# Performance work log

Hardware: AMD Instinct MI355X
Metric: run time of the kernel (lower is better)

Reference implementation:

```python
import jax, jax.numpy as jnp
import numpy as np

H = 768
NH = 12
HD = H // NH
EPS = 1e-12


def setup_inputs() -> dict:
    key = jax.random.key(0)
    ks = jax.random.split(key, 12)
    B, S = 4, 1024
    scale = 0.02
    return {
        "hidden_states": jax.random.normal(ks[0], (B, S, H), jnp.float32),
        "rel_pos": jax.random.normal(ks[1], (B, NH, S, S), jnp.float32),
        "rel_2d_pos": jax.random.normal(ks[2], (B, NH, S, S), jnp.float32),
        "Wq": jax.random.normal(ks[3], (H, H), jnp.float32) * scale,
        "bq": jnp.zeros((H,), jnp.float32),
        "Wk": jax.random.normal(ks[4], (H, H), jnp.float32) * scale,
        "bk": jnp.zeros((H,), jnp.float32),
        "Wv": jax.random.normal(ks[5], (H, H), jnp.float32) * scale,
        "bv": jnp.zeros((H,), jnp.float32),
        "Wo": jax.random.normal(ks[6], (H, H), jnp.float32) * scale,
        "bo": jnp.zeros((H,), jnp.float32),
        "ln_g": jnp.ones((H,), jnp.float32),
        "ln_b": jnp.zeros((H,), jnp.float32),
    }


def reference(hidden_states, rel_pos, rel_2d_pos, Wq, bq, Wk, bk, Wv, bv, Wo, bo, ln_g, ln_b):
    B, S, _ = hidden_states.shape
    # qkv projections -> [B, S, NH, HD]
    q = (hidden_states @ Wq + bq).reshape(B, S, NH, HD)
    k = (hidden_states @ Wk + bk).reshape(B, S, NH, HD)
    v = (hidden_states @ Wv + bv).reshape(B, S, NH, HD)
    q = q / jnp.sqrt(jnp.asarray(HD, q.dtype))
    # attention scores [B, NH, S, S] + relative/spatial biases
    scores = jnp.einsum("bshd,bthd->bhst", q, k) + rel_pos + rel_2d_pos
    probs = jax.nn.softmax(scores.astype(jnp.float32), axis=-1).astype(v.dtype)
    # context [B, S, NH, HD] -> [B, S, H]
    ctx = jnp.einsum("bhst,bthd->bshd", probs, v).reshape(B, S, H)
    # self-output: dense + residual + LayerNorm
    y = ctx @ Wo + bo + hidden_states
    mu = jnp.mean(y, axis=-1, keepdims=True)
    var = jnp.mean((y - mu) ** 2, axis=-1, keepdims=True)
    out = (y - mu) * jax.lax.rsqrt(var + EPS) * ln_g + ln_b
    return out
```

## Files before the change

kernel.cpp:

```cpp
#include <hip/hip_runtime.h>

#define H 768
#define NH 12
#define HD 64
#define BB 4
#define SS 1024
#define MM (BB*SS)

typedef __bf16 bf16;
typedef __bf16 bf16x8 __attribute__((ext_vector_type(8)));
typedef __bf16 bf16x4 __attribute__((ext_vector_type(4)));
typedef float  f32x4  __attribute__((ext_vector_type(4)));

static __device__ __forceinline__ f32x4 mfma16(bf16x8 a, bf16x8 b, f32x4 c){
  return __builtin_amdgcn_mfma_f32_16x16x32_bf16(a, b, c, 0, 0, 0);
}

__global__ __launch_bounds__(256) void prep_hs(const float* __restrict__ hs, bf16* __restrict__ hsb){
  size_t i = (size_t)blockIdx.x*256 + threadIdx.x;
  f32x4 v = *(const f32x4*)(hs + i*4);
  bf16x4 o;
  #pragma unroll
  for(int j=0;j<4;j++) o[j] = (bf16)v[j];
  *(bf16x4*)(hsb + i*4) = o;
}

__global__ __launch_bounds__(256) void prep_wt(const float* __restrict__ Wq, const float* __restrict__ Wk,
                                               const float* __restrict__ Wv, const float* __restrict__ Wo,
                                               bf16* __restrict__ oq, bf16* __restrict__ ok,
                                               bf16* __restrict__ ov, bf16* __restrict__ oo){
  int z = blockIdx.z;
  const float* W = (z==0)?Wq:(z==1)?Wk:(z==2)?Wv:Wo;
  bf16* O = (z==0)?oq:(z==1)?ok:(z==2)?ov:oo;
  __shared__ float tile[64][65];
  int t = threadIdx.x;
  int k0 = blockIdx.y*64, n0 = blockIdx.x*64;
  #pragma unroll
  for(int i=0;i<4;i++){
    int idx = i*256+t; int r = idx>>4; int c4 = (idx&15)*4;
    f32x4 v = *(const f32x4*)(W + (size_t)(k0+r)*H + n0 + c4);
    tile[r][c4+0]=v[0]; tile[r][c4+1]=v[1]; tile[r][c4+2]=v[2]; tile[r][c4+3]=v[3];
  }
  __syncthreads();
  #pragma unroll
  for(int i=0;i<4;i++){
    int idx = i*256+t; int r = idx>>4; int c4 = (idx&15)*4;
    bf16x4 o;
    #pragma unroll
    for(int j=0;j<4;j++) o[j] = (bf16)tile[c4+j][r];
    *(bf16x4*)(O + (size_t)(n0+r)*H + k0 + c4) = o;
  }
}

__global__ __launch_bounds__(256) void qkv_gemm(const bf16* __restrict__ hsb,
    const bf16* __restrict__ wqT, const bf16* __restrict__ wkT, const bf16* __restrict__ wvT,
    const float* __restrict__ bq, const float* __restrict__ bk, const float* __restrict__ bv,
    bf16* __restrict__ qb, bf16* __restrict__ kb, bf16* __restrict__ vb){
  int t = threadIdx.x;
  int m0 = blockIdx.x*64;
  int by = blockIdx.y;
  int mat = by/12, nb = by%12, n0 = nb*64;
  const bf16* wT   = (mat==0)?wqT:(mat==1)?wkT:wvT;
  const float* bias= (mat==0)?bq :(mat==1)?bk :bv;
  bf16* outp       = (mat==0)?qb :(mat==1)?kb :vb;
  float scale      = (mat==0)?0.125f:1.0f;

  __shared__ __align__(16) bf16 As[64*40];
  __shared__ __align__(16) bf16 Bs[64*40];
  int lane=t&63, w=t>>6, g=lane>>4, c=lane&15;
  f32x4 acc[4] = {};
  int ar = t>>2, asg = (t&3)*8;
  for(int kt=0; kt<24; kt++){
    __syncthreads();
    *(bf16x8*)&As[ar*40+asg] = *(const bf16x8*)(hsb + (size_t)(m0+ar)*H + kt*32 + asg);
    *(bf16x8*)&Bs[ar*40+asg] = *(const bf16x8*)(wT  + (size_t)(n0+ar)*H + kt*32 + asg);
    __syncthreads();
    bf16x8 a = *(const bf16x8*)&As[(16*w+c)*40 + g*8];
    #pragma unroll
    for(int ct=0;ct<4;ct++){
      bf16x8 b = *(const bf16x8*)&Bs[(16*ct+c)*40 + g*8];
      acc[ct] = mfma16(a, b, acc[ct]);
    }
  }
  #pragma unroll
  for(int ct=0;ct<4;ct++){
    #pragma unroll
    for(int r=0;r<4;r++){
      int row = m0 + 16*w + 4*g + r;
      int col = 16*ct + c;
      float val = (acc[ct][r] + bias[n0+col]) * scale;
      int b_ = row>>10, s = row&1023;
      outp[(((size_t)(b_*NH + nb))*SS + s)*HD + col] = (bf16)val;
    }
  }
}

__global__ __launch_bounds__(256,3) void attn_kernel(const bf16* __restrict__ qbuf,
    const bf16* __restrict__ kbuf, const bf16* __restrict__ vbuf,
    const float* __restrict__ relp, const float* __restrict__ rel2,
    bf16* __restrict__ ctxb){
  int t = threadIdx.x;
  int qt = blockIdx.x, h = blockIdx.y, b_ = blockIdx.z;
  int q0 = qt*64;
  const bf16* qh = qbuf + ((size_t)(b_*NH+h))*SS*HD;
  const bf16* kh = kbuf + ((size_t)(b_*NH+h))*SS*HD;
  const bf16* vh = vbuf + ((size_t)(b_*NH+h))*SS*HD;
  const float* r1 = relp + ((size_t)(b_*NH+h))*SS*SS;
  const float* r2 = rel2 + ((size_t)(b_*NH+h))*SS*SS;

  __shared__ __align__(16) bf16 Ks[64*64];
  __shared__ __align__(16) bf16 Vs[64*64];
  __shared__ __align__(16) bf16 Ps[4][1024];

  int lane=t&63, w=t>>6, g=lane>>4, c=lane&15;

  bf16x8 aq[2];
  {
    int qrow = q0 + 16*w + c;
    aq[0] = *(const bf16x8*)(qh + (size_t)qrow*HD + g*8);
    aq[1] = *(const bf16x8*)(qh + (size_t)qrow*HD + 32 + g*8);
  }

  const float* p1 = r1 + (size_t)(q0 + 16*w + 4*g)*SS + c;
  const float* p2 = r2 + (size_t)(q0 + 16*w + 4*g)*SS + c;

  int ks_s = t>>3, ks_seg = t&7;
  int ks_lds = ks_s*64 + ((ks_seg ^ (ks_s&7))<<3);

  float rn1[16], rn2[16];
  bf16x8 kreg[2], vreg[2];

  kreg[0] = *(const bf16x8*)(kh + (size_t)ks_s*HD + ks_seg*8);
  kreg[1] = *(const bf16x8*)(kh + (size_t)(32+ks_s)*HD + ks_seg*8);
  vreg[0] = *(const bf16x8*)(vh + (size_t)lane*HD + w*8);
  vreg[1] = *(const bf16x8*)(vh + (size_t)lane*HD + (4+w)*8);
  #pragma unroll
  for(int ct=0;ct<4;ct++)
    #pragma unroll
    for(int r=0;r<4;r++){
      rn1[ct*4+r] = p1[(size_t)r*SS + 16*ct];
      rn2[ct*4+r] = p2[(size_t)r*SS + 16*ct];
    }

  f32x4 cacc[4] = {};
  float m_r[4], l_r[4];
  #pragma unroll
  for(int r=0;r<4;r++){ m_r[r] = -1e30f; l_r[r] = 0.f; }

  for(int kt=0; kt<16; kt++){
    int k0n = (kt<15) ? (kt+1)*64 : kt*64;

    *(bf16x8*)&Ks[ks_lds]         = kreg[0];
    *(bf16x8*)&Ks[32*64 + ks_lds] = kreg[1];
    #pragma unroll
    for(int j=0;j<8;j++){
      Vs[(w*8+j)*64     + (lane ^ (j<<3))] = vreg[0][j];
      Vs[((4+w)*8+j)*64 + (lane ^ (j<<3))] = vreg[1][j];
    }
    kreg[0] = *(const bf16x8*)(kh + (size_t)(k0n+ks_s)*HD + ks_seg*8);
    kreg[1] = *(const bf16x8*)(kh + (size_t)(k0n+32+ks_s)*HD + ks_seg*8);
    vreg[0] = *(const bf16x8*)(vh + (size_t)(k0n+lane)*HD + w*8);
    vreg[1] = *(const bf16x8*)(vh + (size_t)(k0n+lane)*HD + (4+w)*8);

    asm volatile("s_waitcnt lgkmcnt(0)" ::: "memory");
    __builtin_amdgcn_s_barrier();

    float relC[16];
    #pragma unroll
    for(int i=0;i<16;i++) relC[i] = rn1[i] + rn2[i];
    #pragma unroll
    for(int ct=0;ct<4;ct++)
      #pragma unroll
      for(int r=0;r<4;r++){
        rn1[ct*4+r] = p1[(size_t)r*SS + k0n + 16*ct];
        rn2[ct*4+r] = p2[(size_t)r*SS + k0n + 16*ct];
      }

    f32x4 sc[4] = {};
    #pragma unroll
    for(int ks=0; ks<2; ks++){
      #pragma unroll
      for(int ct=0;ct<4;ct++){
        int scol = 16*ct + c;
        int seg = g + 4*ks;
        bf16x8 bk_ = *(const bf16x8*)&Ks[scol*64 + ((seg ^ (scol&7))<<3)];
        sc[ct] = mfma16(aq[ks], bk_, sc[ct]);
      }
    }
    #pragma unroll
    for(int ct=0;ct<4;ct++)
      #pragma unroll
      for(int r=0;r<4;r++)
        sc[ct][r] += relC[ct*4+r];

    #pragma unroll
    for(int r=0;r<4;r++){
      float mv = fmaxf(fmaxf(sc[0][r],sc[1][r]), fmaxf(sc[2][r],sc[3][r]));
      #pragma unroll
      for(int mk=1; mk<16; mk<<=1) mv = fmaxf(mv, __shfl_xor(mv, mk));
      float mn = fmaxf(m_r[r], mv);
      float corr = __expf(m_r[r] - mn);
      m_r[r] = mn;
      float ssum = 0.f;
      #pragma unroll
      for(int ct=0;ct<4;ct++){ float p = __expf(sc[ct][r]-mn); sc[ct][r]=p; ssum += p; }
      #pragma unroll
      for(int mk=1; mk<16; mk<<=1) ssum += __shfl_xor(ssum, mk);
      l_r[r] = l_r[r]*corr + ssum;
      #pragma unroll
      for(int ct=0;ct<4;ct++) cacc[ct][r] *= corr;
    }
    #pragma unroll
    for(int ct=0;ct<4;ct++)
      #pragma unroll
      for(int r=0;r<4;r++){
        int row = 4*g + r, col = 16*ct + c;
        Ps[w][row*64 + (col ^ ((row&7)<<3))] = (bf16)sc[ct][r];
      }
    #pragma unroll
    for(int ks=0;ks<2;ks++){
      int seg = g + 4*ks;
      bf16x8 pa = *(const bf16x8*)&Ps[w][c*64 + ((seg ^ (c&7))<<3)];
      #pragma unroll
      for(int ct=0;ct<4;ct++){
        int d = 16*ct + c;
        bf16x8 bv_ = *(const bf16x8*)&Vs[d*64 + ((seg ^ (d&7))<<3)];
        cacc[ct] = mfma16(pa, bv_, cacc[ct]);
      }
    }
    __builtin_amdgcn_s_barrier();
  }

  #pragma unroll
  for(int ct=0;ct<4;ct++)
    #pragma unroll
    for(int r=0;r<4;r++){
      int row = q0 + 16*w + 4*g + r;
      int col = 16*ct + c;
      float o = cacc[ct][r] / l_r[r];
      ctxb[((size_t)(b_*SS + row))*H + h*HD + col] = (bf16)o;
    }
}

__global__ __launch_bounds__(256) void out_gemm(const bf16* __restrict__ ctxb, const bf16* __restrict__ woT,
    const float* __restrict__ bo, const float* __restrict__ hs, float* __restrict__ y){
  int t = threadIdx.x;
  int m0 = blockIdx.x*64, n0 = blockIdx.y*64;
  __shared__ __align__(16) bf16 As[64*40];
  __shared__ __align__(16) bf16 Bs[64*40];
  int lane=t&63, w=t>>6, g=lane>>4, c=lane&15;
  f32x4 acc[4] = {};
  int ar = t>>2, asg = (t&3)*8;
  for(int kt=0; kt<24; kt++){
    __syncthreads();
    *(bf16x8*)&As[ar*40+asg] = *(const bf16x8*)(ctxb + (size_t)(m0+ar)*H + kt*32 + asg);
    *(bf16x8*)&Bs[ar*40+asg] = *(const bf16x8*)(woT  + (size_t)(n0+ar)*H + kt*32 + asg);
    __syncthreads();
    bf16x8 a = *(const bf16x8*)&As[(16*w+c)*40 + g*8];
    #pragma unroll
    for(int ct=0;ct<4;ct++){
      bf16x8 b = *(const bf16x8*)&Bs[(16*ct+c)*40 + g*8];
      acc[ct] = mfma16(a, b, acc[ct]);
    }
  }
  #pragma unroll
  for(int ct=0;ct<4;ct++)
    #pragma unroll
    for(int r=0;r<4;r++){
      int row = m0 + 16*w + 4*g + r;
      int col = n0 + 16*ct + c;
      y[(size_t)row*H + col] = acc[ct][r] + bo[col] + hs[(size_t)row*H + col];
    }
}

__global__ __launch_bounds__(256) void ln_kernel(const float* __restrict__ y,
    const float* __restrict__ gw, const float* __restrict__ bw, float* __restrict__ out){
  int row = blockIdx.x; int t = threadIdx.x;
  const float* yr = y + (size_t)row*H;
  float v0 = yr[t], v1 = yr[t+256], v2 = yr[t+512];
  float s = v0+v1+v2;
  #pragma unroll
  for(int mk=1; mk<64; mk<<=1) s += __shfl_xor(s, mk);
  __shared__ float red[8];
  int w = t>>6, lane = t&63;
  if(lane==0) red[w] = s;
  __syncthreads();
  float mu = (red[0]+red[1]+red[2]+red[3]) * (1.f/768.f);
  float d0=v0-mu, d1=v1-mu, d2=v2-mu;
  float s2 = d0*d0+d1*d1+d2*d2;
  #pragma unroll
  for(int mk=1; mk<64; mk<<=1) s2 += __shfl_xor(s2, mk);
  __syncthreads();
  if(lane==0) red[w] = s2;
  __syncthreads();
  float var = (red[0]+red[1]+red[2]+red[3]) * (1.f/768.f);
  float inv = rsqrtf(var + 1e-12f);
  out[(size_t)row*H + t]     = d0*inv*gw[t]     + bw[t];
  out[(size_t)row*H + t+256] = d1*inv*gw[t+256] + bw[t+256];
  out[(size_t)row*H + t+512] = d2*inv*gw[t+512] + bw[t+512];
}

extern "C" void kernel_launch(void* const* d_in, const int* in_sizes, int n_in,
                              void* d_out, int out_size, void* d_ws, size_t ws_size,
                              hipStream_t stream){
  const float* hs   = (const float*)d_in[0];
  const float* relp = (const float*)d_in[1];
  const float* rel2 = (const float*)d_in[2];
  const float* Wq   = (const float*)d_in[3];
  const float* bq   = (const float*)d_in[4];
  const float* Wk   = (const float*)d_in[5];
  const float* bk   = (const float*)d_in[6];
  const float* Wv   = (const float*)d_in[7];
  const float* bv   = (const float*)d_in[8];
  const float* Wo   = (const float*)d_in[9];
  const float* bo   = (const float*)d_in[10];
  const float* lng  = (const float*)d_in[11];
  const float* lnb  = (const float*)d_in[12];
  float* out = (float*)d_out;

  char* p = (char*)d_ws;
  bf16* hsb = (bf16*)p; p += (size_t)MM*H*2;
  bf16* wqT = (bf16*)p; p += (size_t)H*H*2;
  bf16* wkT = (bf16*)p; p += (size_t)H*H*2;
  bf16* wvT = (bf16*)p; p += (size_t)H*H*2;
  bf16* woT = (bf16*)p; p += (size_t)H*H*2;
  bf16* qbuf = (bf16*)p; p += (size_t)MM*H*2;
  bf16* kbuf = (bf16*)p; p += (size_t)MM*H*2;
  bf16* vbuf = (bf16*)p; p += (size_t)MM*H*2;
  bf16* ctxb = (bf16*)p; p += (size_t)MM*H*2;
  float* y   = (float*)p; p += (size_t)MM*H*4;

  prep_hs<<<dim3((MM*H/4)/256), 256, 0, stream>>>(hs, hsb);
  prep_wt<<<dim3(12,12,4), 256, 0, stream>>>(Wq, Wk, Wv, Wo, wqT, wkT, wvT, woT);
  qkv_gemm<<<dim3(64,36), 256, 0, stream>>>(hsb, wqT, wkT, wvT, bq, bk, bv, qbuf, kbuf, vbuf);
  attn_kernel<<<dim3(16,12,4), 256, 0, stream>>>(qbuf, kbuf, vbuf, relp, rel2, ctxb);
  out_gemm<<<dim3(64,12), 256, 0, stream>>>(ctxb, woT, bo, hs, y);
  ln_kernel<<<dim3(MM), 256, 0, stream>>>(y, lng, lnb, out);
}
```

Baseline: 180.7 us.

## Double-buffer rel-bias prefetch two tiles ahead and add lazy softmax rescaling

The attention kernel now keeps two register buffers for the rel_pos/rel_2d_pos bias values and prefetches them two key tiles ahead, to hide the latency of these large fp32 streams. The online softmax rescale is skipped unless the running max grows by more than a threshold across the wave. Row-sum reductions are deferred to a single shuffle reduction at the end, and the final division becomes a reciprocal multiply. In exchange, register pressure rises, and the lazy-max threshold means exponentials can reach up to e^8 before a rescale.

```diff
diff --git a/kernel.cpp b/kernel.cpp
--- a/kernel.cpp
+++ b/kernel.cpp
@@ -127,7 +127,7 @@
   int ks_s = t>>3, ks_seg = t&7;
   int ks_lds = ks_s*64 + ((ks_seg ^ (ks_s&7))<<3);
 
-  float rn1[16], rn2[16];
+  float rA1[16], rA2[16], rB1[16], rB2[16];
   bf16x8 kreg[2], vreg[2];
 
   kreg[0] = *(const bf16x8*)(kh + (size_t)ks_s*HD + ks_seg*8);
@@ -138,8 +138,10 @@
   for(int ct=0;ct<4;ct++)
     #pragma unroll
     for(int r=0;r<4;r++){
-      rn1[ct*4+r] = p1[(size_t)r*SS + 16*ct];
-      rn2[ct*4+r] = p2[(size_t)r*SS + 16*ct];
+      rA1[ct*4+r] = p1[(size_t)r*SS + 16*ct];
+      rA2[ct*4+r] = p2[(size_t)r*SS + 16*ct];
+      rB1[ct*4+r] = p1[(size_t)r*SS + 64 + 16*ct];
+      rB2[ct*4+r] = p2[(size_t)r*SS + 64 + 16*ct];
     }
 
   f32x4 cacc[4] = {};
@@ -147,97 +149,127 @@
   #pragma unroll
   for(int r=0;r<4;r++){ m_r[r] = -1e30f; l_r[r] = 0.f; }
 
-  for(int kt=0; kt<16; kt++){
-    int k0n = (kt<15) ? (kt+1)*64 : kt*64;
-
-    *(bf16x8*)&Ks[ks_lds]         = kreg[0];
-    *(bf16x8*)&Ks[32*64 + ks_lds] = kreg[1];
-    #pragma unroll
-    for(int j=0;j<8;j++){
-      Vs[(w*8+j)*64     + (lane ^ (j<<3))] = vreg[0][j];
-      Vs[((4+w)*8+j)*64 + (lane ^ (j<<3))] = vreg[1][j];
-    }
-    kreg[0] = *(const bf16x8*)(kh + (size_t)(k0n+ks_s)*HD + ks_seg*8);
-    kreg[1] = *(const bf16x8*)(kh + (size_t)(k0n+32+ks_s)*HD + ks_seg*8);
-    vreg[0] = *(const bf16x8*)(vh + (size_t)(k0n+lane)*HD + w*8);
-    vreg[1] = *(const bf16x8*)(vh + (size_t)(k0n+lane)*HD + (4+w)*8);
-
-    asm volatile("s_waitcnt lgkmcnt(0)" ::: "memory");
-    __builtin_amdgcn_s_barrier();
-
-    float relC[16];
-    #pragma unroll
-    for(int i=0;i<16;i++) relC[i] = rn1[i] + rn2[i];
-    #pragma unroll
-    for(int ct=0;ct<4;ct++)
-      #pragma unroll
-      for(int r=0;r<4;r++){
-        rn1[ct*4+r] = p1[(size_t)r*SS + k0n + 16*ct];
-        rn2[ct*4+r] = p2[(size_t)r*SS + k0n + 16*ct];
-      }
-
-    f32x4 sc[4] = {};
-    #pragma unroll
-    for(int ks=0; ks<2; ks++){
-      #pragma unroll
-      for(int ct=0;ct<4;ct++){
-        int scol = 16*ct + c;
-        int seg = g + 4*ks;
-        bf16x8 bk_ = *(const bf16x8*)&Ks[scol*64 + ((seg ^ (scol&7))<<3)];
-        sc[ct] = mfma16(aq[ks], bk_, sc[ct]);
-      }
-    }
-    #pragma unroll
-    for(int ct=0;ct<4;ct++)
-      #pragma unroll
-      for(int r=0;r<4;r++)
-        sc[ct][r] += relC[ct*4+r];
-
-    #pragma unroll
-    for(int r=0;r<4;r++){
-      float mv = fmaxf(fmaxf(sc[0][r],sc[1][r]), fmaxf(sc[2][r],sc[3][r]));
-      #pragma unroll
-      for(int mk=1; mk<16; mk<<=1) mv = fmaxf(mv, __shfl_xor(mv, mk));
-      float mn = fmaxf(m_r[r], mv);
-      float corr = __expf(m_r[r] - mn);
-      m_r[r] = mn;
-      float ssum = 0.f;
-      #pragma unroll
-      for(int ct=0;ct<4;ct++){ float p = __expf(sc[ct][r]-mn); sc[ct][r]=p; ssum += p; }
-      #pragma unroll
-      for(int mk=1; mk<16; mk<<=1) ssum += __shfl_xor(ssum, mk);
-      l_r[r] = l_r[r]*corr + ssum;
-      #pragma unroll
-      for(int ct=0;ct<4;ct++) cacc[ct][r] *= corr;
-    }
-    #pragma unroll
-    for(int ct=0;ct<4;ct++)
-      #pragma unroll
-      for(int r=0;r<4;r++){
-        int row = 4*g + r, col = 16*ct + c;
-        Ps[w][row*64 + (col ^ ((row&7)<<3))] = (bf16)sc[ct][r];
-      }
-    #pragma unroll
-    for(int ks=0;ks<2;ks++){
-      int seg = g + 4*ks;
-      bf16x8 pa = *(const bf16x8*)&Ps[w][c*64 + ((seg ^ (c&7))<<3)];
-      #pragma unroll
-      for(int ct=0;ct<4;ct++){
-        int d = 16*ct + c;
-        bf16x8 bv_ = *(const bf16x8*)&Vs[d*64 + ((seg ^ (d&7))<<3)];
-        cacc[ct] = mfma16(pa, bv_, cacc[ct]);
-      }
-    }
-    __builtin_amdgcn_s_barrier();
-  }
-
+#define TILE_BODY(RX1, RX2, KT)                                                 \
+  {                                                                             \
+    int kt_ = (KT);                                                             \
+    int knext = (kt_<15) ? (kt_+1)*64 : kt_*64;                                 \
+    int kpf   = (kt_<14) ? (kt_+2)*64 : kt_*64;                                 \
+                                         \
+    *(bf16x8*)&Ks[ks_lds]         = kreg[0];                                    \
+    *(bf16x8*)&Ks[32*64 + ks_lds] = kreg[1];                                    \
+    _Pragma("unroll")                                                           \
+    for(int j=0;j<8;j++){                                                       \
+      Vs[(w*8+j)*64     + (lane ^ (j<<3))] = vreg[0][j];                        \
+      Vs[((4+w)*8+j)*64 + (lane ^ (j<<3))] = vreg[1][j];                        \
+    }                                                                           \
+                                             \
+    kreg[0] = *(const bf16x8*)(kh + (size_t)(knext+ks_s)*HD + ks_seg*8);        \
+    kreg[1] = *(const bf16x8*)(kh + (size_t)(knext+32+ks_s)*HD + ks_seg*8);     \
+    vreg[0] = *(const bf16x8*)(vh + (size_t)(knext+lane)*HD + w*8);             \
+    vreg[1] = *(const bf16x8*)(vh + (size_t)(knext+lane)*HD + (4+w)*8);         \
+    asm volatile("s_waitcnt lgkmcnt(0)" ::: "memory");                          \
+    __builtin_amdgcn_s_barrier();                                               \
+                                                       \
+    float relC[16];                                                             \
+    _Pragma("unroll")                                                           \
+    for(int i=0;i<16;i++) relC[i] = RX1[i] + RX2[i];                            \
+                                             \
+    _Pragma("unroll")                                                           \
+    for(int ct=0;ct<4;ct++)                                                     \
+      _Pragma("unroll")                                                         \
+      for(int r=0;r<4;r++){                                                     \
+        RX1[ct*4+r] = p1[(size_t)r*SS + kpf + 16*ct];                           \
+        RX2[ct*4+r] = p2[(size_t)r*SS + kpf + 16*ct];                           \
+      }                                                                         \
+                                                                      \
+    f32x4 sc[4] = {};                                                           \
+    _Pragma("unroll")                                                           \
+    for(int ks=0; ks<2; ks++){                                                  \
+      _Pragma("unroll")                                                         \
+      for(int ct=0;ct<4;ct++){                                                  \
+        int scol = 16*ct + c;                                                   \
+        int seg = g + 4*ks;                                                     \
+        bf16x8 bk_ = *(const bf16x8*)&Ks[scol*64 + ((seg ^ (scol&7))<<3)];      \
+        sc[ct] = mfma16(aq[ks], bk_, sc[ct]);                                   \
+      }                                                                         \
+    }                                                                           \
+    _Pragma("unroll")                                                           \
+    for(int ct=0;ct<4;ct++)                                                     \
+      _Pragma("unroll")                                                         \
+      for(int r=0;r<4;r++)                                                      \
+        sc[ct][r] += relC[ct*4+r];                                              \
+                    \
+    float mv[4];                                                                \
+    _Pragma("unroll")                                                           \
+    for(int r=0;r<4;r++){                                                       \
+      float m2 = fmaxf(fmaxf(sc[0][r],sc[1][r]), fmaxf(sc[2][r],sc[3][r]));     \
+      _Pragma("unroll")                                                         \
+      for(int mk=1; mk<16; mk<<=1) m2 = fmaxf(m2, __shfl_xor(m2, mk));          \
+      mv[r] = m2;                                                               \
+    }                                                                           \
+    float grow = fmaxf(fmaxf(mv[0]-m_r[0], mv[1]-m_r[1]),                       \
+                       fmaxf(mv[2]-m_r[2], mv[3]-m_r[3]));                      \
+    if(!__all(grow <= 8.0f)){                                                   \
+      _Pragma("unroll")                                                         \
+      for(int r=0;r<4;r++){                                                     \
+        float mn = fmaxf(m_r[r], mv[r]);                                        \
+        float corr = __expf(m_r[r] - mn);                                       \
+        m_r[r] = mn;                                                            \
+        l_r[r] *= corr;                                                         \
+        _Pragma("unroll")                                                       \
+        for(int ct=0;ct<4;ct++) cacc[ct][r] *= corr;                            \
+      }                                                                         \
+    }                                                                           \
+    _Pragma("unroll")                                                           \
+    for(int r=0;r<4;r++){                                                       \
+      float ls = 0.f;                                                           \
+      _Pragma("unroll")                                                         \
+      for(int ct=0;ct<4;ct++){ float pp = __expf(sc[ct][r]-m_r[r]); sc[ct][r]=pp; ls += pp; } \
+      l_r[r] += ls;                                                             \
+    }                                                                           \
+                                                         \
+    _Pragma("unroll")                                                           \
+    for(int ct=0;ct<4;ct++)                                                     \
+      _Pragma("unroll")                                                         \
+      for(int r=0;r<4;r++){                                                     \
+        int row = 4*g + r, col = 16*ct + c;                                     \
+        Ps[w][row*64 + (col ^ ((row&7)<<3))] = (bf16)sc[ct][r];                 \
+      }                                                                         \
+                                                                        \
+    _Pragma("unroll")                                                           \
+    for(int ks=0;ks<2;ks++){                                                    \
+      int seg = g + 4*ks;                                                       \
+      bf16x8 pa = *(const bf16x8*)&Ps[w][c*64 + ((seg ^ (c&7))<<3)];            \
+      _Pragma("unroll")                                                         \
+      for(int ct=0;ct<4;ct++){                                                  \
+        int d = 16*ct + c;                                                      \
+        bf16x8 bv_ = *(const bf16x8*)&Vs[d*64 + ((seg ^ (d&7))<<3)];            \
+        cacc[ct] = mfma16(pa, bv_, cacc[ct]);                                   \
+      }                                                                         \
+    }                                                                           \
+    __builtin_amdgcn_s_barrier();                                               \
+  }
+
+  for(int i=0; i<8; i++){
+    TILE_BODY(rA1, rA2, 2*i)
+    TILE_BODY(rB1, rB2, 2*i+1)
+  }
+#undef TILE_BODY
+
+  #pragma unroll
+  for(int r=0;r<4;r++){
+    float ls = l_r[r];
+    #pragma unroll
+    for(int mk=1; mk<16; mk<<=1) ls += __shfl_xor(ls, mk);
+    l_r[r] = 1.f/ls;
+  }
   #pragma unroll
   for(int ct=0;ct<4;ct++)
     #pragma unroll
     for(int r=0;r<4;r++){
       int row = q0 + 16*w + 4*g + r;
       int col = 16*ct + c;
-      float o = cacc[ct][r] / l_r[r];
+      float o = cacc[ct][r] * l_r[r];
       ctxb[((size_t)(b_*SS + row))*H + h*HD + col] = (bf16)o;
     }
 }
```

Measured after the change: 461.6 us. +155.4%, slower.

## Stage relative-position bias through LDS with vectorized loads and lazy softmax rescale

Applied to the files above, without the earlier changes.

Each thread now loads the two rel-pos bias tiles as coalesced float4 rows, sums them, and writes them to a shared-memory tile. MFMA-layout threads then read that tile instead of issuing strided scalar global loads. The online softmax also skips the rescale unless some row's max grows by more than 8, and it defers the row-sum shuffle reduction to the end of the kernel. This trades extra LDS space (about 17KB, which may lower occupancy) and a possible overflow risk from the skipped rescale for fewer, wider global loads and less per-tile reduction work.

```diff
diff --git a/kernel.cpp b/kernel.cpp
--- a/kernel.cpp
+++ b/kernel.cpp
@@ -111,6 +111,7 @@
   __shared__ __align__(16) bf16 Ks[64*64];
   __shared__ __align__(16) bf16 Vs[64*64];
   __shared__ __align__(16) bf16 Ps[4][1024];
+  __shared__ __align__(16) float relS[64][68];
 
   int lane=t&63, w=t>>6, g=lane>>4, c=lane&15;
 
@@ -121,13 +122,14 @@
     aq[1] = *(const bf16x8*)(qh + (size_t)qrow*HD + 32 + g*8);
   }
 
-  const float* p1 = r1 + (size_t)(q0 + 16*w + 4*g)*SS + c;
-  const float* p2 = r2 + (size_t)(q0 + 16*w + 4*g)*SS + c;
+  int srow = t>>4, scol = (t&15)*4;
+  const float* p1 = r1 + (size_t)(q0 + srow)*SS + scol;
+  const float* p2 = r2 + (size_t)(q0 + srow)*SS + scol;
 
   int ks_s = t>>3, ks_seg = t&7;
   int ks_lds = ks_s*64 + ((ks_seg ^ (ks_s&7))<<3);
 
-  float rn1[16], rn2[16];
+  f32x4 rr1[4], rr2[4];
   bf16x8 kreg[2], vreg[2];
 
   kreg[0] = *(const bf16x8*)(kh + (size_t)ks_s*HD + ks_seg*8);
@@ -135,12 +137,10 @@
   vreg[0] = *(const bf16x8*)(vh + (size_t)lane*HD + w*8);
   vreg[1] = *(const bf16x8*)(vh + (size_t)lane*HD + (4+w)*8);
   #pragma unroll
-  for(int ct=0;ct<4;ct++)
-    #pragma unroll
-    for(int r=0;r<4;r++){
-      rn1[ct*4+r] = p1[(size_t)r*SS + 16*ct];
-      rn2[ct*4+r] = p2[(size_t)r*SS + 16*ct];
-    }
+  for(int i=0;i<4;i++){
+    rr1[i] = *(const f32x4*)(p1 + (size_t)i*16*SS);
+    rr2[i] = *(const f32x4*)(p2 + (size_t)i*16*SS);
+  }
 
   f32x4 cacc[4] = {};
   float m_r[4], l_r[4];
@@ -148,8 +148,13 @@
   for(int r=0;r<4;r++){ m_r[r] = -1e30f; l_r[r] = 0.f; }
 
   for(int kt=0; kt<16; kt++){
-    int k0n = (kt<15) ? (kt+1)*64 : kt*64;
-
+    int knext = (kt<15 ? kt+1 : 15)*64;
+
+    #pragma unroll
+    for(int i=0;i<4;i++){
+      f32x4 s = rr1[i] + rr2[i];
+      *(f32x4*)&relS[i*16 + srow][scol] = s;
+    }
     *(bf16x8*)&Ks[ks_lds]         = kreg[0];
     *(bf16x8*)&Ks[32*64 + ks_lds] = kreg[1];
     #pragma unroll
@@ -157,33 +162,29 @@
       Vs[(w*8+j)*64     + (lane ^ (j<<3))] = vreg[0][j];
       Vs[((4+w)*8+j)*64 + (lane ^ (j<<3))] = vreg[1][j];
     }
-    kreg[0] = *(const bf16x8*)(kh + (size_t)(k0n+ks_s)*HD + ks_seg*8);
-    kreg[1] = *(const bf16x8*)(kh + (size_t)(k0n+32+ks_s)*HD + ks_seg*8);
-    vreg[0] = *(const bf16x8*)(vh + (size_t)(k0n+lane)*HD + w*8);
-    vreg[1] = *(const bf16x8*)(vh + (size_t)(k0n+lane)*HD + (4+w)*8);
+
+    kreg[0] = *(const bf16x8*)(kh + (size_t)(knext+ks_s)*HD + ks_seg*8);
+    kreg[1] = *(const bf16x8*)(kh + (size_t)(knext+32+ks_s)*HD + ks_seg*8);
+    vreg[0] = *(const bf16x8*)(vh + (size_t)(knext+lane)*HD + w*8);
+    vreg[1] = *(const bf16x8*)(vh + (size_t)(knext+lane)*HD + (4+w)*8);
+    #pragma unroll
+    for(int i=0;i<4;i++){
+      rr1[i] = *(const f32x4*)(p1 + (size_t)i*16*SS + knext);
+      rr2[i] = *(const f32x4*)(p2 + (size_t)i*16*SS + knext);
+    }
+    __builtin_amdgcn_sched_barrier(0);
 
     asm volatile("s_waitcnt lgkmcnt(0)" ::: "memory");
     __builtin_amdgcn_s_barrier();
 
-    float relC[16];
-    #pragma unroll
-    for(int i=0;i<16;i++) relC[i] = rn1[i] + rn2[i];
-    #pragma unroll
-    for(int ct=0;ct<4;ct++)
-      #pragma unroll
-      for(int r=0;r<4;r++){
-        rn1[ct*4+r] = p1[(size_t)r*SS + k0n + 16*ct];
-        rn2[ct*4+r] = p2[(size_t)r*SS + k0n + 16*ct];
-      }
-
     f32x4 sc[4] = {};
     #pragma unroll
     for(int ks=0; ks<2; ks++){
       #pragma unroll
       for(int ct=0;ct<4;ct++){
-        int scol = 16*ct + c;
+        int scol_ = 16*ct + c;
         int seg = g + 4*ks;
-        bf16x8 bk_ = *(const bf16x8*)&Ks[scol*64 + ((seg ^ (scol&7))<<3)];
+        bf16x8 bk_ = *(const bf16x8*)&Ks[scol_*64 + ((seg ^ (scol_&7))<<3)];
         sc[ct] = mfma16(aq[ks], bk_, sc[ct]);
       }
     }
@@ -191,24 +192,35 @@
     for(int ct=0;ct<4;ct++)
       #pragma unroll
       for(int r=0;r<4;r++)
-        sc[ct][r] += relC[ct*4+r];
-
-    #pragma unroll
-    for(int r=0;r<4;r++){
-      float mv = fmaxf(fmaxf(sc[0][r],sc[1][r]), fmaxf(sc[2][r],sc[3][r]));
-      #pragma unroll
-      for(int mk=1; mk<16; mk<<=1) mv = fmaxf(mv, __shfl_xor(mv, mk));
-      float mn = fmaxf(m_r[r], mv);
-      float corr = __expf(m_r[r] - mn);
-      m_r[r] = mn;
-      float ssum = 0.f;
-      #pragma unroll
-      for(int ct=0;ct<4;ct++){ float p = __expf(sc[ct][r]-mn); sc[ct][r]=p; ssum += p; }
-      #pragma unroll
-      for(int mk=1; mk<16; mk<<=1) ssum += __shfl_xor(ssum, mk);
-      l_r[r] = l_r[r]*corr + ssum;
-      #pragma unroll
-      for(int ct=0;ct<4;ct++) cacc[ct][r] *= corr;
+        sc[ct][r] += relS[16*w + 4*g + r][16*ct + c];
+
+    float mv[4];
+    #pragma unroll
+    for(int r=0;r<4;r++){
+      float m2 = fmaxf(fmaxf(sc[0][r],sc[1][r]), fmaxf(sc[2][r],sc[3][r]));
+      #pragma unroll
+      for(int mk=1; mk<16; mk<<=1) m2 = fmaxf(m2, __shfl_xor(m2, mk));
+      mv[r] = m2;
+    }
+    float grow = fmaxf(fmaxf(mv[0]-m_r[0], mv[1]-m_r[1]),
+                       fmaxf(mv[2]-m_r[2], mv[3]-m_r[3]));
+    if(!__all(grow <= 8.0f)){
+      #pragma unroll
+      for(int r=0;r<4;r++){
+        float mn = fmaxf(m_r[r], mv[r]);
+        float corr = __expf(m_r[r] - mn);
+        m_r[r] = mn;
+        l_r[r] *= corr;
+        #pragma unroll
+        for(int ct=0;ct<4;ct++) cacc[ct][r] *= corr;
+      }
+    }
+    #pragma unroll
+    for(int r=0;r<4;r++){
+      float ls = 0.f;
+      #pragma unroll
+      for(int ct=0;ct<4;ct++){ float pp = __expf(sc[ct][r]-m_r[r]); sc[ct][r]=pp; ls += pp; }
+      l_r[r] += ls;
     }
     #pragma unroll
     for(int ct=0;ct<4;ct++)
@@ -232,12 +244,19 @@
   }
 
   #pragma unroll
+  for(int r=0;r<4;r++){
+    float ls = l_r[r];
+    #pragma unroll
+    for(int mk=1; mk<16; mk<<=1) ls += __shfl_xor(ls, mk);
+    l_r[r] = 1.f/ls;
+  }
+  #pragma unroll
   for(int ct=0;ct<4;ct++)
     #pragma unroll
     for(int r=0;r<4;r++){
       int row = q0 + 16*w + 4*g + r;
       int col = 16*ct + c;
-      float o = cacc[ct][r] / l_r[r];
+      float o = cacc[ct][r] * l_r[r];
       ctxb[((size_t)(b_*SS + row))*H + h*HD + col] = (bf16)o;
     }
 }
```

After: 181.9 us. No clear change (+0.6%).
